# Optimization experiments

Hardware: AMD Instinct MI355X
Metric: run time of the kernel (lower is better)

## Reference

```python
import jax, jax.numpy as jnp
import numpy as np

H = 1024
E = 8
K = 2
N = 16384
LN_EPS = 1e-5


def _layernorm(h, g, b):
    m = jnp.mean(h, axis=-1, keepdims=True)
    v = jnp.mean(jnp.square(h - m), axis=-1, keepdims=True)
    return (h - m) * jax.lax.rsqrt(v + LN_EPS) * g + b


def setup_inputs() -> dict:
    key = jax.random.key(0)
    ks = jax.random.split(key, 8)
    s = 0.02
    return {
        "x": jax.random.normal(ks[0], (N, H), dtype=jnp.float32),
        "Wg": jax.random.normal(ks[1], (H, E), dtype=jnp.float32) * s,
        "bg": jnp.zeros((E,), dtype=jnp.float32),
        "W1": jax.random.normal(ks[2], (E, H, H), dtype=jnp.float32) * s,
        "b1": jnp.zeros((E, H), dtype=jnp.float32),
        "g1": jnp.ones((E, H), dtype=jnp.float32),
        "be1": jnp.zeros((E, H), dtype=jnp.float32),
        "W2": jax.random.normal(ks[3], (E, H, H), dtype=jnp.float32) * s,
        "b2": jnp.zeros((E, H), dtype=jnp.float32),
        "g2": jnp.ones((E, H), dtype=jnp.float32),
        "be2": jnp.zeros((E, H), dtype=jnp.float32),
    }


def reference(x, Wg, bg, W1, b1, g1, be1, W2, b2, g2, be2):
    # Gating: softmax over experts, top-k, renormalize
    gate_probs = jax.nn.softmax(x @ Wg + bg, axis=1)            # [N, E]
    tk_p, tk_i = jax.lax.top_k(gate_probs, K)                    # [N, K]
    tk_p = tk_p / (jnp.sum(tk_p, axis=1, keepdims=True) + 1e-9)
    # Dense per-expert combine weight (zero where expert not selected)
    w = jnp.sum(tk_p[:, :, None] * jax.nn.one_hot(tk_i, E, dtype=x.dtype), axis=1)  # [N, E]

    # ResidualBlock per expert, computed densely for all tokens (dropout = eval/no-op)
    h = jnp.einsum('nh,eho->eno', x, W1) + b1[:, None, :]        # [E, N, H]
    h = jax.nn.relu(_layernorm(h, g1[:, None, :], be1[:, None, :]))
    h = jnp.einsum('enh,eho->eno', h, W2) + b2[:, None, :]
    h = _layernorm(h, g2[:, None, :], be2[:, None, :])
    y = jax.nn.relu(x[None, :, :] + h)                           # [E, N, H]

    moe_out = jnp.einsum('ne,enh->nh', w, y)                     # [N, H]
    return moe_out, gate_probs
```

## Files before the change

### kernel.cpp

```cpp
#include <hip/hip_runtime.h>
#include <cstdint>
#include <cstddef>

constexpr int H_DIM = 1024;
constexpr int NE    = 8;
constexpr int NT    = 16384;
constexpr int NP    = NT * 2;

constexpr int BM = 128, BN = 128, BK = 32;
constexpr int NKT = H_DIM / BK;
constexpr int MAX_WG = (NP / BM + NE) * (H_DIM / BN);

typedef __attribute__((ext_vector_type(8))) short          short8;
typedef __attribute__((ext_vector_type(8))) unsigned short ushort8;
typedef __attribute__((ext_vector_type(4))) float          f32x4;

__device__ __forceinline__ unsigned short f2bf(float f) {
  union { float f; uint32_t u; } c; c.f = f;
  uint32_t u = c.u;
  u = (u + 0x7fffu + ((u >> 16) & 1u)) >> 16;
  return (unsigned short)u;
}
__device__ __forceinline__ float bf2f(unsigned short h) {
  union { uint32_t u; float f; } c; c.u = ((uint32_t)h) << 16;
  return c.f;
}

__device__ __forceinline__ void gload16(const unsigned short* g, unsigned short* l) {
  __builtin_amdgcn_global_load_lds((const __attribute__((address_space(1))) void*)g,
                                   (__attribute__((address_space(3))) void*)l, 16, 0, 0);
}

__global__ __launch_bounds__(256) void transpose_convert_kernel(
    const float* __restrict__ W1, const float* __restrict__ W2,
    unsigned short* __restrict__ T1, unsigned short* __restrict__ T2)
{
  __shared__ float tile[64][65];
  int zi = blockIdx.z;
  const float* W = (zi < 8) ? W1 : W2;
  unsigned short* T = (zi < 8) ? T1 : T2;
  int e  = zi & 7;
  int o0 = blockIdx.x * 64;
  int h0 = blockIdx.y * 64;
  int c  = threadIdx.x & 63;
  int r0 = (threadIdx.x >> 6) * 16;
  const float* src = W + ((size_t)e * H_DIM + h0) * H_DIM + o0;
#pragma unroll
  for (int i = 0; i < 16; ++i)
    tile[r0 + i][c] = src[(size_t)(r0 + i) * H_DIM + c];
  __syncthreads();
  unsigned short* dst = T + ((size_t)e * H_DIM + o0) * H_DIM + h0;
#pragma unroll
  for (int i = 0; i < 16; ++i)
    dst[(size_t)(r0 + i) * H_DIM + c] = f2bf(tile[c][r0 + i]);
}

__global__ __launch_bounds__(256) void xgate_kernel(
    const float* __restrict__ X, const float* __restrict__ Wg,
    const float* __restrict__ bg, unsigned short* __restrict__ Xb,
    float* __restrict__ gate_out, int* __restrict__ tk_e, float* __restrict__ tk_w)
{
  int wid = threadIdx.x >> 6, lane = threadIdx.x & 63;
  int n = blockIdx.x * 4 + wid;
  const float* xr = X + (size_t)n * H_DIM;

  const float4* xp = (const float4*)(xr + lane * 16);
  float4 f0 = xp[0], f1 = xp[1], f2 = xp[2], f3 = xp[3];
  float v[16] = {f0.x,f0.y,f0.z,f0.w, f1.x,f1.y,f1.z,f1.w,
                 f2.x,f2.y,f2.z,f2.w, f3.x,f3.y,f3.z,f3.w};

  ushort8 u0, u1;
#pragma unroll
  for (int j = 0; j < 8; ++j) { u0[j] = f2bf(v[j]); u1[j] = f2bf(v[8 + j]); }
  ushort8* xb = (ushort8*)(Xb + (size_t)n * H_DIM + lane * 16);
  xb[0] = u0; xb[1] = u1;

  float acc[8];
#pragma unroll
  for (int e = 0; e < 8; ++e) acc[e] = 0.f;
#pragma unroll
  for (int j = 0; j < 16; ++j) {
    int h = lane * 16 + j;
    const float4* wg = (const float4*)(Wg + (size_t)h * 8);
    float4 a = wg[0], b = wg[1];
    float xv = v[j];
    acc[0] += xv * a.x; acc[1] += xv * a.y; acc[2] += xv * a.z; acc[3] += xv * a.w;
    acc[4] += xv * b.x; acc[5] += xv * b.y; acc[6] += xv * b.z; acc[7] += xv * b.w;
  }
#pragma unroll
  for (int m = 1; m < 64; m <<= 1) {
#pragma unroll
    for (int e = 0; e < 8; ++e) acc[e] += __shfl_xor(acc[e], m);
  }
#pragma unroll
  for (int e = 0; e < 8; ++e) acc[e] += bg[e];

  float mx = acc[0];
#pragma unroll
  for (int e = 1; e < 8; ++e) mx = fmaxf(mx, acc[e]);
  float g[8], s = 0.f;
#pragma unroll
  for (int e = 0; e < 8; ++e) { g[e] = __expf(acc[e] - mx); s += g[e]; }
  float inv = 1.f / s;
#pragma unroll
  for (int e = 0; e < 8; ++e) g[e] *= inv;

  int e0 = 0; float b0 = g[0];
#pragma unroll
  for (int e = 1; e < 8; ++e) if (g[e] > b0) { b0 = g[e]; e0 = e; }
  int e1 = -1; float b1v = -1.f;
#pragma unroll
  for (int e = 0; e < 8; ++e) if (e != e0 && g[e] > b1v) { b1v = g[e]; e1 = e; }
  float s2 = b0 + b1v + 1e-9f;

  if (lane == 0) {
    float4* gp = (float4*)(gate_out + (size_t)n * 8);
    gp[0] = make_float4(g[0], g[1], g[2], g[3]);
    gp[1] = make_float4(g[4], g[5], g[6], g[7]);
    tk_e[2 * n] = e0; tk_e[2 * n + 1] = e1;
    tk_w[2 * n] = b0 / s2; tk_w[2 * n + 1] = b1v / s2;
  }
}

__global__ __launch_bounds__(256) void hist_kernel(
    const int* __restrict__ tk_e, int* __restrict__ blockHist)
{
  __shared__ int h[8];
  if (threadIdx.x < 8) h[threadIdx.x] = 0;
  __syncthreads();
  int i0 = blockIdx.x * 512 + threadIdx.x;
  atomicAdd(&h[tk_e[i0]], 1);
  atomicAdd(&h[tk_e[i0 + 256]], 1);
  __syncthreads();
  if (threadIdx.x < 8) blockHist[blockIdx.x * 8 + threadIdx.x] = h[threadIdx.x];
}

__global__ void scan_kernel(const int* __restrict__ blockHist,
                            int* __restrict__ blockBase,
                            int* __restrict__ count, int* __restrict__ offs)
{
  int e = threadIdx.x;
  if (e < 8) {
    int run = 0;
    for (int b = 0; b < 64; ++b) { blockBase[b * 8 + e] = run; run += blockHist[b * 8 + e]; }
    count[e] = run;
  }
  __syncthreads();
  if (threadIdx.x == 0) {
    int o = 0;
    for (int k = 0; k < 8; ++k) { offs[k] = o; o += count[k]; }
  }
  __syncthreads();
  if (e < 8) {
    int o = offs[e];
    for (int b = 0; b < 64; ++b) blockBase[b * 8 + e] += o;
  }
}

__global__ __launch_bounds__(256) void place_kernel(
    const int* __restrict__ tk_e, const int* __restrict__ blockBase,
    int* __restrict__ pairTok, int* __restrict__ pairExp, int* __restrict__ slots)
{
  __shared__ int cur[8];
  if (threadIdx.x < 8) cur[threadIdx.x] = blockBase[blockIdx.x * 8 + threadIdx.x];
  __syncthreads();
#pragma unroll
  for (int j = 0; j < 2; ++j) {
    int i = blockIdx.x * 512 + j * 256 + threadIdx.x;
    int e = tk_e[i];
    int s = atomicAdd(&cur[e], 1);
    pairTok[s] = i >> 1; pairExp[s] = e; slots[i] = s;
  }
}

__global__ void worklist_kernel(const int* __restrict__ count,
                                int* __restrict__ wl, int* __restrict__ wlCount)
{
  __shared__ int nmt[8], ebase[8], totalS;
  if (threadIdx.x == 0) {
    int o = 0;
    for (int e = 0; e < 8; ++e) {
      nmt[e] = (count[e] + BM - 1) / BM;
      ebase[e] = o;
      o += nmt[e] * (H_DIM / BN);
    }
    totalS = o;
    wlCount[0] = o;
  }
  __syncthreads();
  int total = totalS;
  for (int i = threadIdx.x; i < total; i += blockDim.x) {
    int e = 0;
    while (e < 7 && i >= ebase[e + 1]) ++e;
    int loc = i - ebase[e];
    int nt = loc / nmt[e];
    int mt = loc - nt * nmt[e];
    wl[i] = (e << 20) | (nt << 16) | mt;
  }
}

template<bool GATHER>
__global__ __launch_bounds__(256, 3) void gemm3_kernel(
    const unsigned short* __restrict__ Ab,
    const unsigned short* __restrict__ Bt,
    const float* __restrict__ bias,
    const int* __restrict__ pairTok,
    const int* __restrict__ count, const int* __restrict__ offs,
    const int* __restrict__ wl, const int* __restrict__ wlCount,
    unsigned short* __restrict__ Out)
{
  __shared__ unsigned short As[3 * 4096];
  __shared__ unsigned short Bs[3 * 4096];

  const int total = wlCount[0];
  const int orig = blockIdx.x;
  if (orig >= total) return;
  const int qq = total >> 3, rr = total & 7;
  const int xcd = orig & 7, sub = orig >> 3;
  const int idx = (xcd < rr ? xcd * (qq + 1) : rr * (qq + 1) + (xcd - rr) * qq) + sub;
  const int ent = wl[idx];
  const int e = ent >> 20, ntb = (ent >> 16) & 15, mtb = ent & 0xffff;
  const int cnt = count[e], base = offs[e];

  const int tid = threadIdx.x;
  const int wid = tid >> 6, l = tid & 63;
  const int wr = wid >> 1, wc = wid & 1;

  const int rsub = (l >> 2);
  const int kswz = ((l & 3) * 8) ^ (((l >> 5) & 1) << 4);

  const unsigned short *apg0, *apg1, *bpg0, *bpg1;
  {
    int r0 = wid * 16 + rsub;
    int r1 = 64 + wid * 16 + rsub;
    int g0 = mtb * BM + r0; if (g0 >= cnt) g0 = cnt - 1;
    int g1 = mtb * BM + r1; if (g1 >= cnt) g1 = cnt - 1;
    size_t a0, a1;
    if (GATHER) { a0 = (size_t)pairTok[base + g0]; a1 = (size_t)pairTok[base + g1]; }
    else        { a0 = (size_t)(base + g0);        a1 = (size_t)(base + g1); }
    apg0 = Ab + a0 * H_DIM + kswz;
    apg1 = Ab + a1 * H_DIM + kswz;
    const unsigned short* bb = Bt + ((size_t)e * H_DIM + ntb * BN) * H_DIM + kswz;
    bpg0 = bb + (size_t)r0 * H_DIM;
    bpg1 = bb + (size_t)r1 * H_DIM;
  }

  const int loff = ((l & 15) * 64 + (l >> 4) * 16) ^ (((l >> 3) & 1) << 5);

  auto STAGE = [&](int u, int sl) {
    unsigned short* ad = As + sl * 4096 + wid * 512;
    unsigned short* bd = Bs + sl * 4096 + wid * 512;
    gload16(apg0 + (size_t)u * BK, ad);
    gload16(apg1 + (size_t)u * BK, ad + 2048);
    gload16(bpg0 + (size_t)u * BK, bd);
    gload16(bpg1 + (size_t)u * BK, bd + 2048);
  };

  STAGE(0, 0); STAGE(1, 1);
  asm volatile("s_waitcnt vmcnt(4)" ::: "memory");
  __builtin_amdgcn_s_barrier();

  f32x4 acc[4][4] = {};

  int sl = 0, sstage = 2;
  for (int t = 0; t < NKT; ++t) {
    const char* aB = (const char*)As + sl * 8192 + wr * 4096 + loff;
    const char* bB = (const char*)Bs + sl * 8192 + wc * 4096 + loff;

    short8 af[4], bfr[4];
#pragma unroll
    for (int j = 0; j < 4; ++j) af[j] = *(const short8*)(aB + j * 1024);
#pragma unroll
    for (int r = 0; r < 4; ++r) bfr[r] = *(const short8*)(bB + r * 1024);

    if (t + 2 < NKT) STAGE(t + 2, sstage);

    __builtin_amdgcn_s_setprio(1);
#pragma unroll
    for (int j = 0; j < 4; ++j)
#pragma unroll
      for (int r = 0; r < 4; ++r)
        acc[j][r] = __builtin_amdgcn_mfma_f32_16x16x32_bf16(af[j], bfr[r], acc[j][r], 0, 0, 0);
    __builtin_amdgcn_s_setprio(0);

    if (t + 2 < NKT)      asm volatile("s_waitcnt vmcnt(4)" ::: "memory");
    else if (t + 2 == NKT) asm volatile("s_waitcnt vmcnt(0)" ::: "memory");
    __builtin_amdgcn_s_barrier();

    sl = (sl == 2) ? 0 : sl + 1;
    sstage = (sstage == 2) ? 0 : sstage + 1;
  }

  float bvv[4];
#pragma unroll
  for (int r = 0; r < 4; ++r)
    bvv[r] = bias[e * H_DIM + ntb * BN + wc * 64 + r * 16 + (l & 15)];
#pragma unroll
  for (int j = 0; j < 4; ++j) {
    int grow0 = mtb * BM + wr * 64 + j * 16 + (l >> 4) * 4;
#pragma unroll
    for (int r = 0; r < 4; ++r) {
      int gcol = ntb * BN + wc * 64 + r * 16 + (l & 15);
#pragma unroll
      for (int v = 0; v < 4; ++v) {
        int row = grow0 + v;
        if (row < cnt)
          Out[(size_t)(base + row) * H_DIM + gcol] = f2bf(acc[j][r][v] + bvv[r]);
      }
    }
  }
}

__global__ __launch_bounds__(256) void ln_relu_kernel(
    unsigned short* __restrict__ buf, const float* __restrict__ gamma,
    const float* __restrict__ beta, const int* __restrict__ pairExp)
{
  int wid = threadIdx.x >> 6, lane = threadIdx.x & 63;
  int row = blockIdx.x * 4 + wid;
  int e = pairExp[row];
  unsigned short* r = buf + (size_t)row * H_DIM;
  ushort8 u0 = ((const ushort8*)r)[lane];
  ushort8 u1 = ((const ushort8*)r)[lane + 64];
  float v[16];
#pragma unroll
  for (int j = 0; j < 8; ++j) { v[j] = bf2f(u0[j]); v[8 + j] = bf2f(u1[j]); }
  float s = 0.f, ss = 0.f;
#pragma unroll
  for (int j = 0; j < 16; ++j) { s += v[j]; ss += v[j] * v[j]; }
#pragma unroll
  for (int m = 1; m < 64; m <<= 1) { s += __shfl_xor(s, m); ss += __shfl_xor(ss, m); }
  float mean = s * (1.f / 1024.f);
  float var  = ss * (1.f / 1024.f) - mean * mean;
  float rs   = rsqrtf(var + 1e-5f);

  int h0 = lane * 8, h1 = 512 + lane * 8;
  const float4* gp0 = (const float4*)(gamma + (size_t)e * H_DIM + h0);
  const float4* bp0 = (const float4*)(beta  + (size_t)e * H_DIM + h0);
  const float4* gp1 = (const float4*)(gamma + (size_t)e * H_DIM + h1);
  const float4* bp1 = (const float4*)(beta  + (size_t)e * H_DIM + h1);
  float4 ga = gp0[0], gb = gp0[1], gc = gp1[0], gd = gp1[1];
  float4 ba = bp0[0], bb = bp0[1], bc = bp1[0], bd = bp1[1];
  float gv[16] = {ga.x,ga.y,ga.z,ga.w, gb.x,gb.y,gb.z,gb.w,
                  gc.x,gc.y,gc.z,gc.w, gd.x,gd.y,gd.z,gd.w};
  float bv[16] = {ba.x,ba.y,ba.z,ba.w, bb.x,bb.y,bb.z,bb.w,
                  bc.x,bc.y,bc.z,bc.w, bd.x,bd.y,bd.z,bd.w};
#pragma unroll
  for (int j = 0; j < 8; ++j) {
    float t0 = fmaxf((v[j]     - mean) * rs * gv[j]     + bv[j],     0.f);
    float t1 = fmaxf((v[8 + j] - mean) * rs * gv[8 + j] + bv[8 + j], 0.f);
    u0[j] = f2bf(t0); u1[j] = f2bf(t1);
  }
  ((ushort8*)r)[lane] = u0; ((ushort8*)r)[lane + 64] = u1;
}

__global__ __launch_bounds__(256) void combine_kernel(
    const unsigned short* __restrict__ buf2, const float* __restrict__ X,
    const float* __restrict__ g2, const float* __restrict__ be2,
    const int* __restrict__ slots, const int* __restrict__ tk_e,
    const float* __restrict__ tk_w, float* __restrict__ out)
{
  int wid = threadIdx.x >> 6, lane = threadIdx.x & 63;
  int n = blockIdx.x * 4 + wid;
  int h0 = lane * 8, h1 = 512 + lane * 8;

  const float4* xp0 = (const float4*)(X + (size_t)n * H_DIM + h0);
  const float4* xp1 = (const float4*)(X + (size_t)n * H_DIM + h1);
  float4 xa = xp0[0], xb = xp0[1], xc = xp1[0], xd = xp1[1];
  float xv[16] = {xa.x,xa.y,xa.z,xa.w, xb.x,xb.y,xb.z,xb.w,
                  xc.x,xc.y,xc.z,xc.w, xd.x,xd.y,xd.z,xd.w};
  float o[16];
#pragma unroll
  for (int j = 0; j < 16; ++j) o[j] = 0.f;

#pragma unroll
  for (int k = 0; k < 2; ++k) {
    int slot = slots[2 * n + k];
    int e = tk_e[2 * n + k];
    float w = tk_w[2 * n + k];
    const unsigned short* r = buf2 + (size_t)slot * H_DIM;
    ushort8 u0 = ((const ushort8*)r)[lane];
    ushort8 u1 = ((const ushort8*)r)[lane + 64];
    float v[16];
#pragma unroll
    for (int j = 0; j < 8; ++j) { v[j] = bf2f(u0[j]); v[8 + j] = bf2f(u1[j]); }
    float s = 0.f, ss = 0.f;
#pragma unroll
    for (int j = 0; j < 16; ++j) { s += v[j]; ss += v[j] * v[j]; }
#pragma unroll
    for (int m = 1; m < 64; m <<= 1) { s += __shfl_xor(s, m); ss += __shfl_xor(ss, m); }
    float mean = s * (1.f / 1024.f);
    float var  = ss * (1.f / 1024.f) - mean * mean;
    float rs   = rsqrtf(var + 1e-5f);

    const float4* gp0 = (const float4*)(g2  + (size_t)e * H_DIM + h0);
    const float4* bp0 = (const float4*)(be2 + (size_t)e * H_DIM + h0);
    const float4* gp1 = (const float4*)(g2  + (size_t)e * H_DIM + h1);
    const float4* bp1 = (const float4*)(be2 + (size_t)e * H_DIM + h1);
    float4 ga = gp0[0], gb = gp0[1], gc = gp1[0], gd = gp1[1];
    float4 ba = bp0[0], bb = bp0[1], bc = bp1[0], bd = bp1[1];
    float gv[16] = {ga.x,ga.y,ga.z,ga.w, gb.x,gb.y,gb.z,gb.w,
                    gc.x,gc.y,gc.z,gc.w, gd.x,gd.y,gd.z,gd.w};
    float bvv[16] = {ba.x,ba.y,ba.z,ba.w, bb.x,bb.y,bb.z,bb.w,
                     bc.x,bc.y,bc.z,bc.w, bd.x,bd.y,bd.z,bd.w};
#pragma unroll
    for (int j = 0; j < 16; ++j) {
      float u = (v[j] - mean) * rs * gv[j] + bvv[j];
      float y = fmaxf(xv[j] + u, 0.f);
      o[j] += w * y;
    }
  }

  float4* op0 = (float4*)(out + (size_t)n * H_DIM + h0);
  float4* op1 = (float4*)(out + (size_t)n * H_DIM + h1);
  op0[0] = make_float4(o[0], o[1], o[2], o[3]);
  op0[1] = make_float4(o[4], o[5], o[6], o[7]);
  op1[0] = make_float4(o[8], o[9], o[10], o[11]);
  op1[1] = make_float4(o[12], o[13], o[14], o[15]);
}

extern "C" void kernel_launch(void* const* d_in, const int* in_sizes, int n_in,
                              void* d_out, int out_size, void* d_ws, size_t ws_size,
                              hipStream_t stream)
{
  const float* x   = (const float*)d_in[0];
  const float* Wg  = (const float*)d_in[1];
  const float* bg  = (const float*)d_in[2];
  const float* W1  = (const float*)d_in[3];
  const float* b1  = (const float*)d_in[4];
  const float* g1  = (const float*)d_in[5];
  const float* be1 = (const float*)d_in[6];
  const float* W2  = (const float*)d_in[7];
  const float* b2  = (const float*)d_in[8];
  const float* g2  = (const float*)d_in[9];
  const float* be2 = (const float*)d_in[10];
  float* out = (float*)d_out;
  float* gate_out = out + (size_t)NT * H_DIM;

  char* ws = (char*)d_ws;
  size_t off = 0;
  auto alloc = [&](size_t bytes) { char* p = ws + off; off += (bytes + 255) & ~(size_t)255; return p; };
  unsigned short* w1bt = (unsigned short*)alloc((size_t)NE * H_DIM * H_DIM * 2);
  unsigned short* w2bt = (unsigned short*)alloc((size_t)NE * H_DIM * H_DIM * 2);
  unsigned short* buf1 = (unsigned short*)alloc((size_t)NP * H_DIM * 2);
  unsigned short* buf2 = (unsigned short*)alloc((size_t)NP * H_DIM * 2);
  int*   tk_e      = (int*)alloc((size_t)NP * 4);
  float* tk_w      = (float*)alloc((size_t)NP * 4);
  int*   pairTok   = (int*)alloc((size_t)NP * 4);
  int*   pairExp   = (int*)alloc((size_t)NP * 4);
  int*   slots     = (int*)alloc((size_t)NP * 4);
  int*   blockHist = (int*)alloc(64 * 8 * 4);
  int*   blockBase = (int*)alloc(64 * 8 * 4);
  int*   count     = (int*)alloc(8 * 4);
  int*   offs      = (int*)alloc(8 * 4);
  int*   wl        = (int*)alloc(MAX_WG * 4);
  int*   wlCount   = (int*)alloc(4);
  (void)in_sizes; (void)n_in; (void)out_size; (void)ws_size;

  unsigned short* Xb = buf2;

  transpose_convert_kernel<<<dim3(16, 16, 16), 256, 0, stream>>>(W1, W2, w1bt, w2bt);
  xgate_kernel<<<dim3(NT / 4), 256, 0, stream>>>(x, Wg, bg, Xb, gate_out, tk_e, tk_w);
  hist_kernel<<<dim3(64), 256, 0, stream>>>(tk_e, blockHist);
  scan_kernel<<<dim3(1), 64, 0, stream>>>(blockHist, blockBase, count, offs);
  worklist_kernel<<<dim3(1), 256, 0, stream>>>(count, wl, wlCount);
  place_kernel<<<dim3(64), 256, 0, stream>>>(tk_e, blockBase, pairTok, pairExp, slots);
  gemm3_kernel<true><<<dim3(MAX_WG), 256, 0, stream>>>(
      Xb, w1bt, b1, pairTok, count, offs, wl, wlCount, buf1);
  ln_relu_kernel<<<dim3(NP / 4), 256, 0, stream>>>(buf1, g1, be1, pairExp);
  gemm3_kernel<false><<<dim3(MAX_WG), 256, 0, stream>>>(
      buf1, w2bt, b2, pairTok, count, offs, wl, wlCount, buf2);
  combine_kernel<<<dim3(NT / 4), 256, 0, stream>>>(
      buf2, x, g2, be2, slots, tk_e, tk_w, out);
}
```

Baseline: 389.5 us.

## Switch grouped GEMM to 32x32x16 MFMA and merge prep and scan kernels

The grouped expert GEMMs now use 32x32x16 bf16 MFMA instructions with a 2x2 accumulator tile per wave, in place of a 4x4 grid of 16x16x32 instructions. LDS fragment addressing and the epilogue row/column mapping are rewritten to match the new output layout. The aim is fewer LDS fragment loads per MFMA and higher matrix-core throughput. Separately, the weight transpose/convert and the x-gating kernels are merged into one launch, and the scan and worklist kernels are fused, to cut launch overhead. The risks are the changed LDS bank-conflict pattern from the new swizzle offsets and register pressure from the 16-wide accumulators under launch bounds of 3.

New measurement: 392.6 us. Within noise of the previous version (+0.8%).

```diff
diff --git a/kernel.cpp b/kernel.cpp
--- a/kernel.cpp
+++ b/kernel.cpp
@@ -11,9 +11,10 @@
 constexpr int NKT = H_DIM / BK;
 constexpr int MAX_WG = (NP / BM + NE) * (H_DIM / BN);
 
-typedef __attribute__((ext_vector_type(8))) short          short8;
-typedef __attribute__((ext_vector_type(8))) unsigned short ushort8;
-typedef __attribute__((ext_vector_type(4))) float          f32x4;
+typedef __attribute__((ext_vector_type(8)))  short          short8;
+typedef __attribute__((ext_vector_type(8)))  unsigned short ushort8;
+typedef __attribute__((ext_vector_type(4)))  float          f32x4;
+typedef __attribute__((ext_vector_type(16))) float          f32x16;
 
 __device__ __forceinline__ unsigned short f2bf(float f) {
   union { float f; uint32_t u; } c; c.f = f;
@@ -31,37 +32,39 @@
                                    (__attribute__((address_space(3))) void*)l, 16, 0, 0);
 }
 
-__global__ __launch_bounds__(256) void transpose_convert_kernel(
+__global__ __launch_bounds__(256) void prep_kernel(
+    const float* __restrict__ X, const float* __restrict__ Wg,
+    const float* __restrict__ bg, unsigned short* __restrict__ Xb,
+    float* __restrict__ gate_out, int* __restrict__ tk_e, float* __restrict__ tk_w,
     const float* __restrict__ W1, const float* __restrict__ W2,
     unsigned short* __restrict__ T1, unsigned short* __restrict__ T2)
 {
   __shared__ float tile[64][65];
-  int zi = blockIdx.z;
-  const float* W = (zi < 8) ? W1 : W2;
-  unsigned short* T = (zi < 8) ? T1 : T2;
-  int e  = zi & 7;
-  int o0 = blockIdx.x * 64;
-  int h0 = blockIdx.y * 64;
-  int c  = threadIdx.x & 63;
-  int r0 = (threadIdx.x >> 6) * 16;
-  const float* src = W + ((size_t)e * H_DIM + h0) * H_DIM + o0;
-#pragma unroll
-  for (int i = 0; i < 16; ++i)
-    tile[r0 + i][c] = src[(size_t)(r0 + i) * H_DIM + c];
-  __syncthreads();
-  unsigned short* dst = T + ((size_t)e * H_DIM + o0) * H_DIM + h0;
-#pragma unroll
-  for (int i = 0; i < 16; ++i)
-    dst[(size_t)(r0 + i) * H_DIM + c] = f2bf(tile[c][r0 + i]);
-}
-
-__global__ __launch_bounds__(256) void xgate_kernel(
-    const float* __restrict__ X, const float* __restrict__ Wg,
-    const float* __restrict__ bg, unsigned short* __restrict__ Xb,
-    float* __restrict__ gate_out, int* __restrict__ tk_e, float* __restrict__ tk_w)
-{
+  int b = blockIdx.x;
+  if (b >= 4096) {
+    int t = b - 4096;
+    int zi = t >> 8;
+    const float* W = (zi < 8) ? W1 : W2;
+    unsigned short* T = (zi < 8) ? T1 : T2;
+    int e  = zi & 7;
+    int o0 = ((t >> 4) & 15) * 64;
+    int h0 = (t & 15) * 64;
+    int c  = threadIdx.x & 63;
+    int r0 = (threadIdx.x >> 6) * 16;
+    const float* src = W + ((size_t)e * H_DIM + h0) * H_DIM + o0;
+#pragma unroll
+    for (int i = 0; i < 16; ++i)
+      tile[r0 + i][c] = src[(size_t)(r0 + i) * H_DIM + c];
+    __syncthreads();
+    unsigned short* dst = T + ((size_t)e * H_DIM + o0) * H_DIM + h0;
+#pragma unroll
+    for (int i = 0; i < 16; ++i)
+      dst[(size_t)(r0 + i) * H_DIM + c] = f2bf(tile[c][r0 + i]);
+    return;
+  }
+
   int wid = threadIdx.x >> 6, lane = threadIdx.x & 63;
-  int n = blockIdx.x * 4 + wid;
+  int n = b * 4 + wid;
   const float* xr = X + (size_t)n * H_DIM;
 
   const float4* xp = (const float4*)(xr + lane * 16);
@@ -82,10 +85,10 @@
   for (int j = 0; j < 16; ++j) {
     int h = lane * 16 + j;
     const float4* wg = (const float4*)(Wg + (size_t)h * 8);
-    float4 a = wg[0], b = wg[1];
+    float4 a = wg[0], bb = wg[1];
     float xv = v[j];
-    acc[0] += xv * a.x; acc[1] += xv * a.y; acc[2] += xv * a.z; acc[3] += xv * a.w;
-    acc[4] += xv * b.x; acc[5] += xv * b.y; acc[6] += xv * b.z; acc[7] += xv * b.w;
+    acc[0] += xv * a.x;  acc[1] += xv * a.y;  acc[2] += xv * a.z;  acc[3] += xv * a.w;
+    acc[4] += xv * bb.x; acc[5] += xv * bb.y; acc[6] += xv * bb.z; acc[7] += xv * bb.w;
   }
 #pragma unroll
   for (int m = 1; m < 64; m <<= 1) {
@@ -135,10 +138,12 @@
   if (threadIdx.x < 8) blockHist[blockIdx.x * 8 + threadIdx.x] = h[threadIdx.x];
 }
 
-__global__ void scan_kernel(const int* __restrict__ blockHist,
-                            int* __restrict__ blockBase,
-                            int* __restrict__ count, int* __restrict__ offs)
-{
+__global__ void scan_worklist_kernel(const int* __restrict__ blockHist,
+                                     int* __restrict__ blockBase,
+                                     int* __restrict__ count, int* __restrict__ offs,
+                                     int* __restrict__ wl, int* __restrict__ wlCount)
+{
+  __shared__ int nmt[8], ebase[8], totalS;
   int e = threadIdx.x;
   if (e < 8) {
     int run = 0;
@@ -147,13 +152,27 @@
   }
   __syncthreads();
   if (threadIdx.x == 0) {
-    int o = 0;
-    for (int k = 0; k < 8; ++k) { offs[k] = o; o += count[k]; }
+    int o = 0, wo = 0;
+    for (int k = 0; k < 8; ++k) {
+      offs[k] = o; o += count[k];
+      nmt[k] = (count[k] + BM - 1) / BM;
+      ebase[k] = wo; wo += nmt[k] * (H_DIM / BN);
+    }
+    totalS = wo; wlCount[0] = wo;
   }
   __syncthreads();
   if (e < 8) {
     int o = offs[e];
     for (int b = 0; b < 64; ++b) blockBase[b * 8 + e] += o;
+  }
+  int total = totalS;
+  for (int i = threadIdx.x; i < total; i += blockDim.x) {
+    int ee = 0;
+    while (ee < 7 && i >= ebase[ee + 1]) ++ee;
+    int loc = i - ebase[ee];
+    int nt = loc / nmt[ee];
+    int mt = loc - nt * nmt[ee];
+    wl[i] = (ee << 20) | (nt << 16) | mt;
   }
 }
 
@@ -173,34 +192,8 @@
   }
 }
 
-__global__ void worklist_kernel(const int* __restrict__ count,
-                                int* __restrict__ wl, int* __restrict__ wlCount)
-{
-  __shared__ int nmt[8], ebase[8], totalS;
-  if (threadIdx.x == 0) {
-    int o = 0;
-    for (int e = 0; e < 8; ++e) {
-      nmt[e] = (count[e] + BM - 1) / BM;
-      ebase[e] = o;
-      o += nmt[e] * (H_DIM / BN);
-    }
-    totalS = o;
-    wlCount[0] = o;
-  }
-  __syncthreads();
-  int total = totalS;
-  for (int i = threadIdx.x; i < total; i += blockDim.x) {
-    int e = 0;
-    while (e < 7 && i >= ebase[e + 1]) ++e;
-    int loc = i - ebase[e];
-    int nt = loc / nmt[e];
-    int mt = loc - nt * nmt[e];
-    wl[i] = (e << 20) | (nt << 16) | mt;
-  }
-}
-
 template<bool GATHER>
-__global__ __launch_bounds__(256, 3) void gemm3_kernel(
+__global__ __launch_bounds__(256, 3) void gemm32_kernel(
     const unsigned short* __restrict__ Ab,
     const unsigned short* __restrict__ Bt,
     const float* __restrict__ bias,
@@ -245,7 +238,10 @@
     bpg1 = bb + (size_t)r1 * H_DIM;
   }
 
-  const int loff = ((l & 15) * 64 + (l >> 4) * 16) ^ (((l >> 3) & 1) << 5);
+  const int lrow = (l & 15) * 64 + ((l >> 4) & 1) * 1024;
+  const int sw = ((l >> 3) & 1) << 5;
+  const int kb0 = (((l >> 5) * 16) + 0)  ^ sw;
+  const int kb1 = (((l >> 5) * 16) + 32) ^ sw;
 
   auto STAGE = [&](int u, int sl) {
     unsigned short* ad = As + sl * 4096 + wid * 512;
@@ -260,30 +256,35 @@
   asm volatile("s_waitcnt vmcnt(4)" ::: "memory");
   __builtin_amdgcn_s_barrier();
 
-  f32x4 acc[4][4] = {};
+  f32x16 acc[2][2] = {};
 
   int sl = 0, sstage = 2;
   for (int t = 0; t < NKT; ++t) {
-    const char* aB = (const char*)As + sl * 8192 + wr * 4096 + loff;
-    const char* bB = (const char*)Bs + sl * 8192 + wc * 4096 + loff;
-
-    short8 af[4], bfr[4];
-#pragma unroll
-    for (int j = 0; j < 4; ++j) af[j] = *(const short8*)(aB + j * 1024);
-#pragma unroll
-    for (int r = 0; r < 4; ++r) bfr[r] = *(const short8*)(bB + r * 1024);
+    const char* aB = (const char*)As + sl * 8192 + wr * 4096 + lrow;
+    const char* bB = (const char*)Bs + sl * 8192 + wc * 4096 + lrow;
+
+    short8 af[2][2], bf[2][2];
+#pragma unroll
+    for (int j = 0; j < 2; ++j) {
+      af[j][0] = *(const short8*)(aB + j * 2048 + kb0);
+      af[j][1] = *(const short8*)(aB + j * 2048 + kb1);
+      bf[j][0] = *(const short8*)(bB + j * 2048 + kb0);
+      bf[j][1] = *(const short8*)(bB + j * 2048 + kb1);
+    }
 
     if (t + 2 < NKT) STAGE(t + 2, sstage);
 
     __builtin_amdgcn_s_setprio(1);
 #pragma unroll
-    for (int j = 0; j < 4; ++j)
-#pragma unroll
-      for (int r = 0; r < 4; ++r)
-        acc[j][r] = __builtin_amdgcn_mfma_f32_16x16x32_bf16(af[j], bfr[r], acc[j][r], 0, 0, 0);
+    for (int ks = 0; ks < 2; ++ks)
+#pragma unroll
+      for (int j = 0; j < 2; ++j)
+#pragma unroll
+        for (int r = 0; r < 2; ++r)
+          acc[j][r] = __builtin_amdgcn_mfma_f32_32x32x16_bf16(af[j][ks], bf[r][ks], acc[j][r], 0, 0, 0);
     __builtin_amdgcn_s_setprio(0);
 
-    if (t + 2 < NKT)      asm volatile("s_waitcnt vmcnt(4)" ::: "memory");
+    if (t + 2 < NKT)       asm volatile("s_waitcnt vmcnt(4)" ::: "memory");
     else if (t + 2 == NKT) asm volatile("s_waitcnt vmcnt(0)" ::: "memory");
     __builtin_amdgcn_s_barrier();
 
@@ -291,24 +292,22 @@
     sstage = (sstage == 2) ? 0 : sstage + 1;
   }
 
-  float bvv[4];
-#pragma unroll
-  for (int r = 0; r < 4; ++r)
-    bvv[r] = bias[e * H_DIM + ntb * BN + wc * 64 + r * 16 + (l & 15)];
-#pragma unroll
-  for (int j = 0; j < 4; ++j) {
-    int grow0 = mtb * BM + wr * 64 + j * 16 + (l >> 4) * 4;
-#pragma unroll
-    for (int r = 0; r < 4; ++r) {
-      int gcol = ntb * BN + wc * 64 + r * 16 + (l & 15);
-#pragma unroll
-      for (int v = 0; v < 4; ++v) {
-        int row = grow0 + v;
+  float bvv[2];
+#pragma unroll
+  for (int r = 0; r < 2; ++r)
+    bvv[r] = bias[e * H_DIM + ntb * BN + wc * 64 + r * 32 + (l & 31)];
+#pragma unroll
+  for (int j = 0; j < 2; ++j)
+#pragma unroll
+    for (int r = 0; r < 2; ++r) {
+      int gcol = ntb * BN + wc * 64 + r * 32 + (l & 31);
+#pragma unroll
+      for (int reg = 0; reg < 16; ++reg) {
+        int row = mtb * BM + wr * 64 + j * 32 + (reg & 3) + 8 * (reg >> 2) + 4 * (l >> 5);
         if (row < cnt)
-          Out[(size_t)(base + row) * H_DIM + gcol] = f2bf(acc[j][r][v] + bvv[r]);
+          Out[(size_t)(base + row) * H_DIM + gcol] = f2bf(acc[j][r][reg] + bvv[r]);
       }
     }
-  }
 }
 
 __global__ __launch_bounds__(256) void ln_relu_kernel(
@@ -458,16 +457,15 @@
 
   unsigned short* Xb = buf2;
 
-  transpose_convert_kernel<<<dim3(16, 16, 16), 256, 0, stream>>>(W1, W2, w1bt, w2bt);
-  xgate_kernel<<<dim3(NT / 4), 256, 0, stream>>>(x, Wg, bg, Xb, gate_out, tk_e, tk_w);
+  prep_kernel<<<dim3(8192), 256, 0, stream>>>(
+      x, Wg, bg, Xb, gate_out, tk_e, tk_w, W1, W2, w1bt, w2bt);
   hist_kernel<<<dim3(64), 256, 0, stream>>>(tk_e, blockHist);
-  scan_kernel<<<dim3(1), 64, 0, stream>>>(blockHist, blockBase, count, offs);
-  worklist_kernel<<<dim3(1), 256, 0, stream>>>(count, wl, wlCount);
+  scan_worklist_kernel<<<dim3(1), 256, 0, stream>>>(blockHist, blockBase, count, offs, wl, wlCount);
   place_kernel<<<dim3(64), 256, 0, stream>>>(tk_e, blockBase, pairTok, pairExp, slots);
-  gemm3_kernel<true><<<dim3(MAX_WG), 256, 0, stream>>>(
+  gemm32_kernel<true><<<dim3(MAX_WG), 256, 0, stream>>>(
       Xb, w1bt, b1, pairTok, count, offs, wl, wlCount, buf1);
   ln_relu_kernel<<<dim3(NP / 4), 256, 0, stream>>>(buf1, g1, be1, pairExp);
-  gemm3_kernel<false><<<dim3(MAX_WG), 256, 0, stream>>>(
+  gemm32_kernel<false><<<dim3(MAX_WG), 256, 0, stream>>>(
       buf1, w2bt, b2, pairTok, count, offs, wl, wlCount, buf2);
   combine_kernel<<<dim3(NT / 4), 256, 0, stream>>>(
       buf2, x, g2, be2, slots, tk_e, tk_w, out);
```
